# Kernel tuning notes

Hardware: AMD Instinct MI355X
Metric: run time of the kernel (lower is better)

## Reference

```python
import jax, jax.numpy as jnp
import numpy as np

B, G, FI, FO, H, W = 16, 8, 64, 64, 64, 64
N_ITER = 3


def setup_inputs() -> dict:
    key = jax.random.key(0)
    kx, kw, kb = jax.random.split(key, 3)
    x = jax.random.normal(kx, (B, G * FI, H, W), dtype=jnp.float32)
    # kaiming_normal_ on [fo*g, fi, 1, 1]: std = sqrt(2 / fan_in), fan_in = fi*1*1
    weight = jax.random.normal(kw, (FO * G, FI, 1, 1), dtype=jnp.float32) * np.sqrt(2.0 / FI)
    bias = jax.random.normal(kb, (1, FO, 1, 1), dtype=jnp.float32) * 0.01
    return {"x": x, "weight": weight, "bias": bias}


def reference(x, weight, bias):
    g, n_iter = G, N_ITER
    gfo, fi = weight.shape[:2]
    fo = gfo // g
    b, c, h, w = x.shape
    # grouped 1x1 conv == per-group channel matmul
    xg = x.reshape(b, g, fi, h, w)
    wg = weight.reshape(g, fo, fi)
    con = jnp.einsum('bgihw,gfi->bgfhw', xg, wg)  # [B, g, fo, H, W]
    beta = jnp.zeros((), dtype=x.dtype)
    for i in range(n_iter):
        alpha = jax.nn.sigmoid(beta)
        v = jnp.sum(alpha * con, axis=1, keepdims=True)  # [B, 1, fo, H, W]
        if i == n_iter - 1:
            out = v[:, 0]  # [B, fo, H, W]
            return out + bias
        beta = beta + jnp.sum(v * con, axis=2, keepdims=True)  # [B, g, 1, H, W]
```

## Files before the change

### kernel.cpp

```cpp
#include <hip/hip_runtime.h>


typedef __attribute__((ext_vector_type(8))) _Float16 half8;
typedef __attribute__((ext_vector_type(4))) float f32x4;

#define NG   8
#define NFI  64
#define NFO  64
#define HW   4096

__device__ __forceinline__ float sigmoidf_fast(float v) {
    float e = __builtin_amdgcn_exp2f(-1.44269504088896f * v);
    return __builtin_amdgcn_rcpf(1.0f + e);
}

__global__ __launch_bounds__(256)
void wconv_kernel(const float* __restrict__ w, _Float16* __restrict__ wbuf) {
    int V = blockIdx.x * 256 + threadIdx.x;
    int g    = V >> 10;
    int t    = (V >> 8) & 3;
    int c    = (V >> 6) & 3;
    int lane = V & 63;
    int pl = lane & 15, q = lane >> 4;
    const float* src = w + g * (NFO * NFI) + (t * 16 + pl) * NFI + (c & 1) * 32 + q * 8;
    half8 o;
    #pragma unroll
    for (int j = 0; j < 8; ++j) {
        float f = src[j];
        _Float16 h = (_Float16)f;
        o[j] = (c >> 1) ? (_Float16)(f - (float)h) : h;
    }
    *(half8*)(wbuf + (size_t)V * 8) = o;
}

__global__ __launch_bounds__(256, 2)
void routing_kernel(const float* __restrict__ x,
                    const _Float16* __restrict__ wbuf,
                    const float* __restrict__ bias,
                    float* __restrict__ out) {
    const int tid  = threadIdx.x;
    const int b    = blockIdx.x >> 6;
    const int p0   = (blockIdx.x & 63) << 6;
    const int lane = tid & 63;
    const int wv   = tid >> 6;
    const int pl   = lane & 15;
    const int q    = lane >> 4;
    const int pw   = wv * 16 + pl;

    const float* xg = x + (size_t)b * (NG * NFI) * HW + p0 + pw;

    f32x4 acc[NG][4];
    #pragma unroll
    for (int g = 0; g < NG; ++g)
        #pragma unroll
        for (int t = 0; t < 4; ++t)
            acc[g][t] = (f32x4){0.f, 0.f, 0.f, 0.f};

#define XDECL(NM) float NM##0, NM##1, NM##2, NM##3, NM##4, NM##5, NM##6, NM##7, \
                        NM##8, NM##9, NM##10, NM##11, NM##12, NM##13, NM##14, NM##15;
#define XLOAD(G, NM)                                                         \
    {                                                                        \
        const float* p_ = xg + (size_t)((G) * 64 + q * 8) * HW;              \
        NM##0 = p_[(size_t)0 * HW];  NM##1 = p_[(size_t)1 * HW];             \
        NM##2 = p_[(size_t)2 * HW];  NM##3 = p_[(size_t)3 * HW];             \
        NM##4 = p_[(size_t)4 * HW];  NM##5 = p_[(size_t)5 * HW];             \
        NM##6 = p_[(size_t)6 * HW];  NM##7 = p_[(size_t)7 * HW];             \
        const float* p2_ = p_ + (size_t)32 * HW;                             \
        NM##8  = p2_[(size_t)0 * HW]; NM##9  = p2_[(size_t)1 * HW];          \
        NM##10 = p2_[(size_t)2 * HW]; NM##11 = p2_[(size_t)3 * HW];          \
        NM##12 = p2_[(size_t)4 * HW]; NM##13 = p2_[(size_t)5 * HW];          \
        NM##14 = p2_[(size_t)6 * HW]; NM##15 = p2_[(size_t)7 * HW];          \
    }
#define XGRP(G, NM)                                                          \
    {                                                                        \
        half8 b0, b1;                                                        \
        b0[0] = (_Float16)NM##0;  b0[1] = (_Float16)NM##1;                   \
        b0[2] = (_Float16)NM##2;  b0[3] = (_Float16)NM##3;                   \
        b0[4] = (_Float16)NM##4;  b0[5] = (_Float16)NM##5;                   \
        b0[6] = (_Float16)NM##6;  b0[7] = (_Float16)NM##7;                   \
        b1[0] = (_Float16)NM##8;  b1[1] = (_Float16)NM##9;                   \
        b1[2] = (_Float16)NM##10; b1[3] = (_Float16)NM##11;                  \
        b1[4] = (_Float16)NM##12; b1[5] = (_Float16)NM##13;                  \
        b1[6] = (_Float16)NM##14; b1[7] = (_Float16)NM##15;                  \
        const _Float16* wg_ = wbuf + (size_t)(G) * 16 * 512 + lane * 8;      \
        _Pragma("unroll")                                                    \
        for (int t = 0; t < 4; ++t) {                                        \
            const _Float16* wp_ = wg_ + (size_t)t * 2048;                    \
            half8 a0h = *(const half8*)(wp_);                                \
            half8 a1h = *(const half8*)(wp_ + 512);                          \
            half8 a0l = *(const half8*)(wp_ + 1024);                         \
            half8 a1l = *(const half8*)(wp_ + 1536);                         \
            acc[G][t] = __builtin_amdgcn_mfma_f32_16x16x32_f16(a0h, b0, acc[G][t], 0, 0, 0); \
            acc[G][t] = __builtin_amdgcn_mfma_f32_16x16x32_f16(a1h, b1, acc[G][t], 0, 0, 0); \
            acc[G][t] = __builtin_amdgcn_mfma_f32_16x16x32_f16(a0l, b0, acc[G][t], 0, 0, 0); \
            acc[G][t] = __builtin_amdgcn_mfma_f32_16x16x32_f16(a1l, b1, acc[G][t], 0, 0, 0); \
        }                                                                    \
    }

    XDECL(X0) XDECL(X1) XDECL(X2)

    XLOAD(0, X0)
    XLOAD(1, X1)
    XLOAD(2, X2) XGRP(0, X0)
    XLOAD(3, X0) XGRP(1, X1)
    XLOAD(4, X1) XGRP(2, X2)
    XLOAD(5, X2) XGRP(3, X0)
    XLOAD(6, X0) XGRP(4, X1)
    XLOAD(7, X1) XGRP(5, X2)
    XGRP(6, X0)
    XGRP(7, X1)

#undef XDECL
#undef XLOAD
#undef XGRP

    float v0[4][4];
    #pragma unroll
    for (int t = 0; t < 4; ++t)
        #pragma unroll
        for (int r = 0; r < 4; ++r) {
            float s = 0.f;
            #pragma unroll
            for (int g = 0; g < NG; ++g) s += acc[g][t][r];
            v0[t][r] = 0.5f * s;
        }

    float beta[NG], alpha[NG];
    #pragma unroll
    for (int g = 0; g < NG; ++g) {
        float s = 0.f;
        #pragma unroll
        for (int t = 0; t < 4; ++t)
            #pragma unroll
            for (int r = 0; r < 4; ++r)
                s += v0[t][r] * acc[g][t][r];
        s += __shfl_xor(s, 16);
        s += __shfl_xor(s, 32);
        beta[g]  = s;
        alpha[g] = sigmoidf_fast(s);
    }

    #pragma unroll
    for (int t = 0; t < 4; ++t)
        #pragma unroll
        for (int r = 0; r < 4; ++r) {
            float s = 0.f;
            #pragma unroll
            for (int g = 0; g < NG; ++g) s += alpha[g] * acc[g][t][r];
            v0[t][r] = s;
        }
    #pragma unroll
    for (int g = 0; g < NG; ++g) {
        float s = 0.f;
        #pragma unroll
        for (int t = 0; t < 4; ++t)
            #pragma unroll
            for (int r = 0; r < 4; ++r)
                s += v0[t][r] * acc[g][t][r];
        s += __shfl_xor(s, 16);
        s += __shfl_xor(s, 32);
        beta[g] += s;
        alpha[g] = sigmoidf_fast(beta[g]);
    }

    #pragma unroll
    for (int t = 0; t < 4; ++t)
        #pragma unroll
        for (int r = 0; r < 4; ++r) {
            int f = t * 16 + q * 4 + r;
            float s = bias[f];
            #pragma unroll
            for (int g = 0; g < NG; ++g) s += alpha[g] * acc[g][t][r];
            out[((size_t)(b * NFO + f)) * HW + p0 + pw] = s;
        }
}

extern "C" void kernel_launch(void* const* d_in, const int* in_sizes, int n_in,
                              void* d_out, int out_size, void* d_ws, size_t ws_size,
                              hipStream_t stream) {
    const float* x    = (const float*)d_in[0];
    const float* w    = (const float*)d_in[1];
    const float* bias = (const float*)d_in[2];
    float* out = (float*)d_out;
    _Float16* wbuf = (_Float16*)d_ws;

    wconv_kernel<<<32, 256, 0, stream>>>(w, wbuf);
    routing_kernel<<<1024, 256, 0, stream>>>(x, wbuf, bias, out);
}
```

Measured before the change: 210.7 us.

## Recompute grouped conv per routing pass to cut registers and raise occupancy

Instead of holding all 8x4 MFMA accumulators (128 floats per lane) live across the routing iterations, the kernel keeps only the fp16-converted x fragments. It recomputes each group's conv output with MFMAs in each of three streaming passes, folding the reductions group by group. Launch bounds are raised from 2 to 3 blocks per SIMD to use the freed registers for occupancy. The price is three times the MFMA work and weight reloads, traded for less register pressure and better latency hiding on a memory-bound load.

```diff
diff --git a/kernel.cpp b/kernel.cpp
--- a/kernel.cpp
+++ b/kernel.cpp
@@ -33,7 +33,7 @@
     *(half8*)(wbuf + (size_t)V * 8) = o;
 }
 
-__global__ __launch_bounds__(256, 2)
+__global__ __launch_bounds__(256, 3)
 void routing_kernel(const float* __restrict__ x,
                     const _Float16* __restrict__ wbuf,
                     const float* __restrict__ bias,
@@ -49,12 +49,7 @@
 
     const float* xg = x + (size_t)b * (NG * NFI) * HW + p0 + pw;
 
-    f32x4 acc[NG][4];
-    #pragma unroll
-    for (int g = 0; g < NG; ++g)
-        #pragma unroll
-        for (int t = 0; t < 4; ++t)
-            acc[g][t] = (f32x4){0.f, 0.f, 0.f, 0.f};
+    half8 bh[NG][2];
 
 #define XDECL(NM) float NM##0, NM##1, NM##2, NM##3, NM##4, NM##5, NM##6, NM##7, \
                         NM##8, NM##9, NM##10, NM##11, NM##12, NM##13, NM##14, NM##15;
@@ -71,107 +66,126 @@
         NM##12 = p2_[(size_t)4 * HW]; NM##13 = p2_[(size_t)5 * HW];          \
         NM##14 = p2_[(size_t)6 * HW]; NM##15 = p2_[(size_t)7 * HW];          \
     }
-#define XGRP(G, NM)                                                          \
-    {                                                                        \
-        half8 b0, b1;                                                        \
-        b0[0] = (_Float16)NM##0;  b0[1] = (_Float16)NM##1;                   \
-        b0[2] = (_Float16)NM##2;  b0[3] = (_Float16)NM##3;                   \
-        b0[4] = (_Float16)NM##4;  b0[5] = (_Float16)NM##5;                   \
-        b0[6] = (_Float16)NM##6;  b0[7] = (_Float16)NM##7;                   \
-        b1[0] = (_Float16)NM##8;  b1[1] = (_Float16)NM##9;                   \
-        b1[2] = (_Float16)NM##10; b1[3] = (_Float16)NM##11;                  \
-        b1[4] = (_Float16)NM##12; b1[5] = (_Float16)NM##13;                  \
-        b1[6] = (_Float16)NM##14; b1[7] = (_Float16)NM##15;                  \
-        const _Float16* wg_ = wbuf + (size_t)(G) * 16 * 512 + lane * 8;      \
-        _Pragma("unroll")                                                    \
-        for (int t = 0; t < 4; ++t) {                                        \
-            const _Float16* wp_ = wg_ + (size_t)t * 2048;                    \
-            half8 a0h = *(const half8*)(wp_);                                \
-            half8 a1h = *(const half8*)(wp_ + 512);                          \
-            half8 a0l = *(const half8*)(wp_ + 1024);                         \
-            half8 a1l = *(const half8*)(wp_ + 1536);                         \
-            acc[G][t] = __builtin_amdgcn_mfma_f32_16x16x32_f16(a0h, b0, acc[G][t], 0, 0, 0); \
-            acc[G][t] = __builtin_amdgcn_mfma_f32_16x16x32_f16(a1h, b1, acc[G][t], 0, 0, 0); \
-            acc[G][t] = __builtin_amdgcn_mfma_f32_16x16x32_f16(a0l, b0, acc[G][t], 0, 0, 0); \
-            acc[G][t] = __builtin_amdgcn_mfma_f32_16x16x32_f16(a1l, b1, acc[G][t], 0, 0, 0); \
-        }                                                                    \
-    }
-
-    XDECL(X0) XDECL(X1) XDECL(X2)
-
-    XLOAD(0, X0)
-    XLOAD(1, X1)
-    XLOAD(2, X2) XGRP(0, X0)
-    XLOAD(3, X0) XGRP(1, X1)
-    XLOAD(4, X1) XGRP(2, X2)
-    XLOAD(5, X2) XGRP(3, X0)
-    XLOAD(6, X0) XGRP(4, X1)
-    XLOAD(7, X1) XGRP(5, X2)
-    XGRP(6, X0)
-    XGRP(7, X1)
-
+#define XCVT(G, NM)                                                          \
+    {                                                                        \
+        half8 t0, t1;                                                        \
+        t0[0] = (_Float16)NM##0;  t0[1] = (_Float16)NM##1;                   \
+        t0[2] = (_Float16)NM##2;  t0[3] = (_Float16)NM##3;                   \
+        t0[4] = (_Float16)NM##4;  t0[5] = (_Float16)NM##5;                   \
+        t0[6] = (_Float16)NM##6;  t0[7] = (_Float16)NM##7;                   \
+        t1[0] = (_Float16)NM##8;  t1[1] = (_Float16)NM##9;                   \
+        t1[2] = (_Float16)NM##10; t1[3] = (_Float16)NM##11;                  \
+        t1[4] = (_Float16)NM##12; t1[5] = (_Float16)NM##13;                  \
+        t1[6] = (_Float16)NM##14; t1[7] = (_Float16)NM##15;                  \
+        bh[G][0] = t0; bh[G][1] = t1;                                        \
+    }
+
+    XDECL(XA) XDECL(XB)
+    XLOAD(0, XA)
+    XLOAD(1, XB)
+    XCVT(0, XA) XLOAD(2, XA)
+    XCVT(1, XB) XLOAD(3, XB)
+    XCVT(2, XA) XLOAD(4, XA)
+    XCVT(3, XB) XLOAD(5, XB)
+    XCVT(4, XA) XLOAD(6, XA)
+    XCVT(5, XB) XLOAD(7, XB)
+    XCVT(6, XA)
+    XCVT(7, XB)
 #undef XDECL
 #undef XLOAD
-#undef XGRP
-
-    float v0[4][4];
+#undef XCVT
+
+#define CONGT(G, T, CV)                                                      \
+    {                                                                        \
+        const _Float16* wp_ = wbuf + (size_t)(G) * 8192 + (T) * 2048 + lane * 8; \
+        half8 a0h = *(const half8*)(wp_);                                    \
+        half8 a1h = *(const half8*)(wp_ + 512);                              \
+        half8 a0l = *(const half8*)(wp_ + 1024);                             \
+        half8 a1l = *(const half8*)(wp_ + 1536);                             \
+        CV = __builtin_amdgcn_mfma_f32_16x16x32_f16(a0h, bh[G][0], CV, 0, 0, 0); \
+        CV = __builtin_amdgcn_mfma_f32_16x16x32_f16(a1h, bh[G][1], CV, 0, 0, 0); \
+        CV = __builtin_amdgcn_mfma_f32_16x16x32_f16(a0l, bh[G][0], CV, 0, 0, 0); \
+        CV = __builtin_amdgcn_mfma_f32_16x16x32_f16(a1l, bh[G][1], CV, 0, 0, 0); \
+    }
+#define CONG(G)                                                              \
+    c0 = (f32x4){0.f,0.f,0.f,0.f}; c1 = (f32x4){0.f,0.f,0.f,0.f};            \
+    c2 = (f32x4){0.f,0.f,0.f,0.f}; c3 = (f32x4){0.f,0.f,0.f,0.f};            \
+    CONGT(G, 0, c0) CONGT(G, 1, c1) CONGT(G, 2, c2) CONGT(G, 3, c3)
+
+    f32x4 c0, c1, c2, c3;
+
+    f32x4 v0[4];
+    #pragma unroll
+    for (int t = 0; t < 4; ++t) v0[t] = (f32x4){0.f,0.f,0.f,0.f};
+#define PASSA(G)                                                             \
+    {                                                                        \
+        CONG(G)                                                              \
+        _Pragma("unroll")                                                    \
+        for (int r = 0; r < 4; ++r) {                                        \
+            v0[0][r] += c0[r]; v0[1][r] += c1[r];                            \
+            v0[2][r] += c2[r]; v0[3][r] += c3[r];                            \
+        }                                                                    \
+    }
+    PASSA(0) PASSA(1) PASSA(2) PASSA(3) PASSA(4) PASSA(5) PASSA(6) PASSA(7)
     #pragma unroll
     for (int t = 0; t < 4; ++t)
         #pragma unroll
-        for (int r = 0; r < 4; ++r) {
-            float s = 0.f;
-            #pragma unroll
-            for (int g = 0; g < NG; ++g) s += acc[g][t][r];
-            v0[t][r] = 0.5f * s;
-        }
-
-    float beta[NG], alpha[NG];
-    #pragma unroll
-    for (int g = 0; g < NG; ++g) {
-        float s = 0.f;
-        #pragma unroll
-        for (int t = 0; t < 4; ++t)
-            #pragma unroll
-            for (int r = 0; r < 4; ++r)
-                s += v0[t][r] * acc[g][t][r];
-        s += __shfl_xor(s, 16);
-        s += __shfl_xor(s, 32);
-        beta[g]  = s;
-        alpha[g] = sigmoidf_fast(s);
-    }
-
-    #pragma unroll
-    for (int t = 0; t < 4; ++t)
-        #pragma unroll
-        for (int r = 0; r < 4; ++r) {
-            float s = 0.f;
-            #pragma unroll
-            for (int g = 0; g < NG; ++g) s += alpha[g] * acc[g][t][r];
-            v0[t][r] = s;
-        }
-    #pragma unroll
-    for (int g = 0; g < NG; ++g) {
-        float s = 0.f;
-        #pragma unroll
-        for (int t = 0; t < 4; ++t)
-            #pragma unroll
-            for (int r = 0; r < 4; ++r)
-                s += v0[t][r] * acc[g][t][r];
-        s += __shfl_xor(s, 16);
-        s += __shfl_xor(s, 32);
-        beta[g] += s;
-        alpha[g] = sigmoidf_fast(beta[g]);
-    }
+        for (int r = 0; r < 4; ++r) v0[t][r] *= 0.5f;
+
+    float beta[NG];
+    f32x4 v1[4];
+    #pragma unroll
+    for (int t = 0; t < 4; ++t) v1[t] = (f32x4){0.f,0.f,0.f,0.f};
+#define PASSB(G)                                                             \
+    {                                                                        \
+        CONG(G)                                                              \
+        float s = 0.f;                                                       \
+        _Pragma("unroll")                                                    \
+        for (int r = 0; r < 4; ++r)                                          \
+            s += v0[0][r]*c0[r] + v0[1][r]*c1[r] + v0[2][r]*c2[r] + v0[3][r]*c3[r]; \
+        s += __shfl_xor(s, 16); s += __shfl_xor(s, 32);                      \
+        beta[G] = s;                                                         \
+        float al = sigmoidf_fast(s);                                         \
+        _Pragma("unroll")                                                    \
+        for (int r = 0; r < 4; ++r) {                                        \
+            v1[0][r] += al*c0[r]; v1[1][r] += al*c1[r];                      \
+            v1[2][r] += al*c2[r]; v1[3][r] += al*c3[r];                      \
+        }                                                                    \
+    }
+    PASSB(0) PASSB(1) PASSB(2) PASSB(3) PASSB(4) PASSB(5) PASSB(6) PASSB(7)
+
+    f32x4 o[4];
+    #pragma unroll
+    for (int t = 0; t < 4; ++t) o[t] = (f32x4){0.f,0.f,0.f,0.f};
+#define PASSC(G)                                                             \
+    {                                                                        \
+        CONG(G)                                                              \
+        float s = 0.f;                                                       \
+        _Pragma("unroll")                                                    \
+        for (int r = 0; r < 4; ++r)                                          \
+            s += v1[0][r]*c0[r] + v1[1][r]*c1[r] + v1[2][r]*c2[r] + v1[3][r]*c3[r]; \
+        s += __shfl_xor(s, 16); s += __shfl_xor(s, 32);                      \
+        float al = sigmoidf_fast(beta[G] + s);                               \
+        _Pragma("unroll")                                                    \
+        for (int r = 0; r < 4; ++r) {                                        \
+            o[0][r] += al*c0[r]; o[1][r] += al*c1[r];                        \
+            o[2][r] += al*c2[r]; o[3][r] += al*c3[r];                        \
+        }                                                                    \
+    }
+    PASSC(0) PASSC(1) PASSC(2) PASSC(3) PASSC(4) PASSC(5) PASSC(6) PASSC(7)
+
+#undef PASSA
+#undef PASSB
+#undef PASSC
+#undef CONG
+#undef CONGT
 
     #pragma unroll
     for (int t = 0; t < 4; ++t)
         #pragma unroll
         for (int r = 0; r < 4; ++r) {
             int f = t * 16 + q * 4 + r;
-            float s = bias[f];
-            #pragma unroll
-            for (int g = 0; g < NG; ++g) s += alpha[g] * acc[g][t][r];
-            out[((size_t)(b * NFO + f)) * HW + p0 + pw] = s;
+            out[((size_t)(b * NFO + f)) * HW + p0 + pw] = o[t][r] + bias[f];
         }
 }
 
```

New measurement: 228.6 us. 1.09x slower.
